# Kernel tuning notes

Measured on AMD Instinct MI355X. Metric: run time of the kernel, lower is better.

The kernel has to match this reference:

```python
import jax, jax.numpy as jnp
import numpy as np

N = 2097152
RES = 512
N_LEVELS = 6  # 512,256,128,64,32,16 (stop at LIGHT_MIN_RES=16)
MIN_ROUGHNESS = 0.08
MAX_ROUGHNESS = 0.5


def _dot(a, b):
    return jnp.sum(a * b, axis=-1, keepdims=True)


def _safe_normalize(x):
    return x / jnp.sqrt(jnp.clip(_dot(x, x), 1e-20, None))


def _reflect(x, n):
    return 2.0 * _dot(x, n) * n - x


def _rgb_to_srgb(x):
    return jnp.where(x <= 0.0031308, 12.92 * x,
                     1.055 * jnp.power(jnp.maximum(x, 0.0031308), 1.0 / 2.4) - 0.055)


def _cube_face_uv(d):
    # OpenGL / nvdiffrast cube-map convention (inverse of util.cube_to_dir)
    x, y, z = d[..., 0], d[..., 1], d[..., 2]
    ax, ay, az = jnp.abs(x), jnp.abs(y), jnp.abs(z)
    is_x = (ax >= ay) & (ax >= az)
    is_y = (~is_x) & (ay >= az)
    face = jnp.where(is_x, jnp.where(x > 0, 0, 1),
           jnp.where(is_y, jnp.where(y > 0, 2, 3),
                           jnp.where(z > 0, 4, 5)))
    ma = jnp.maximum(jnp.where(is_x, ax, jnp.where(is_y, ay, az)), 1e-20)
    u = jnp.where(is_x, jnp.where(x > 0, -z, z),
        jnp.where(is_y, x, jnp.where(z > 0, x, -x)))
    v = jnp.where(is_y, jnp.where(y > 0, z, -z), -y)
    return face, u / ma, v / ma


def _bilinear_gather(tex, face, fx, fy):
    # tex: [6,H,W,C]; face/fx/fy: [N]
    H, W = tex.shape[1], tex.shape[2]
    x0 = jnp.floor(fx); y0 = jnp.floor(fy)
    tx = (fx - x0)[:, None]; ty = (fy - y0)[:, None]
    x0i = jnp.clip(x0.astype(jnp.int32), 0, W - 1)
    x1i = jnp.clip(x0i + 1, 0, W - 1)
    y0i = jnp.clip(y0.astype(jnp.int32), 0, H - 1)
    y1i = jnp.clip(y0i + 1, 0, H - 1)
    c00 = tex[face, y0i, x0i]; c01 = tex[face, y0i, x1i]
    c10 = tex[face, y1i, x0i]; c11 = tex[face, y1i, x1i]
    return (c00 * (1 - tx) + c01 * tx) * (1 - ty) + (c10 * (1 - tx) + c11 * tx) * ty


def _sample_cubemap(tex, dirs):
    H, W = tex.shape[1], tex.shape[2]
    face, u, v = _cube_face_uv(dirs)
    return _bilinear_gather(tex, face, (u * 0.5 + 0.5) * W - 0.5, (v * 0.5 + 0.5) * H - 0.5)


def _sample_cubemap_mip(mips, dirs, level):
    # trilinear: bilinear in each of the two bracketing mip levels + lerp on level
    L = len(mips)
    samples = jnp.stack([_sample_cubemap(m, dirs) for m in mips], axis=0)  # [L,N,C]
    lvl = jnp.clip(level, 0.0, L - 1.0)
    l0 = jnp.floor(lvl).astype(jnp.int32)
    l1 = jnp.minimum(l0 + 1, L - 1)
    f = (lvl - l0.astype(lvl.dtype))[:, None]
    n = jnp.arange(dirs.shape[0])
    return samples[l0, n] * (1 - f) + samples[l1, n] * f


def _sample_lut(lut, uv):
    # lut: [H,W,C]; uv in [0,1], u -> width, v -> height, clamp boundary
    H, W = lut.shape[0], lut.shape[1]
    fx = uv[:, 0] * W - 0.5; fy = uv[:, 1] * H - 0.5
    x0 = jnp.floor(fx); y0 = jnp.floor(fy)
    tx = (fx - x0)[:, None]; ty = (fy - y0)[:, None]
    x0i = jnp.clip(x0.astype(jnp.int32), 0, W - 1); x1i = jnp.clip(x0i + 1, 0, W - 1)
    y0i = jnp.clip(y0.astype(jnp.int32), 0, H - 1); y1i = jnp.clip(y0i + 1, 0, H - 1)
    c00 = lut[y0i, x0i]; c01 = lut[y0i, x1i]; c10 = lut[y1i, x0i]; c11 = lut[y1i, x1i]
    return (c00 * (1 - tx) + c01 * tx) * (1 - ty) + (c10 * (1 - tx) + c11 * tx) * ty


def _get_mip(roughness, n_levels):
    lo = (jnp.clip(roughness, MIN_ROUGHNESS, MAX_ROUGHNESS) - MIN_ROUGHNESS) \
         / (MAX_ROUGHNESS - MIN_ROUGHNESS) * (n_levels - 2)
    hi = (jnp.clip(roughness, MAX_ROUGHNESS, 1.0) - MAX_ROUGHNESS) / (1.0 - MAX_ROUGHNESS) + n_levels - 2
    return jnp.where(roughness < MAX_ROUGHNESS, lo, hi)


def _shade(view_dir, normal, kd, ks, reflect_occ, diffuse_map, mips, fg_lut):
    roughness = ks[:, 1:2]
    metallic = ks[:, 2:3]
    spec_col = (1.0 - metallic) * 0.04 + kd * metallic
    diff_col = kd * (1.0 - metallic)
    reflvec = _safe_normalize(_reflect(view_dir, normal))
    diffuse = jnp.clip(_sample_cubemap(diffuse_map, normal), 0.0, None)
    shaded = diffuse * diff_col * (1.0 - ks[:, 0:1])
    NdotV = jnp.clip(_dot(view_dir, normal), 1e-4, None)
    fg = _sample_lut(fg_lut, jnp.concatenate([NdotV, roughness], axis=-1))
    miplevel = _get_mip(roughness[:, 0], len(mips))
    spec = jnp.clip(_sample_cubemap_mip(mips, reflvec, miplevel), 0.0, None)
    reflectance = spec_col * fg[:, 0:1] + fg[:, 1:2]
    shaded = shaded + spec * reflectance * (1.0 - reflect_occ)
    return _rgb_to_srgb(jnp.clip(shaded, 0.0, 1.0))


def setup_inputs() -> dict:
    key = jax.random.key(0)
    k = jax.random.split(key, 16)
    inp = {
        "view_dir": _safe_normalize(jax.random.normal(k[0], (N, 3), jnp.float32)),
        "normal": _safe_normalize(jax.random.normal(k[1], (N, 3), jnp.float32)),
        "kd": jax.random.uniform(k[2], (N, 3), jnp.float32),
        "ks": jax.random.uniform(k[3], (N, 3), jnp.float32),
        "reflect_occ": jax.random.uniform(k[4], (N, 1), jnp.float32),
    }
    # learned / prefiltered environment light parameters (from build_mips)
    inp["diffuse_map"] = jax.random.uniform(k[5], (6, 16, 16, 3), jnp.float32)
    res = RES
    for i in range(N_LEVELS):
        inp[f"spec{i}"] = jax.random.uniform(k[6 + i], (6, res, res, 3), jnp.float32)
        res //= 2
    inp["fg_lut"] = jax.random.uniform(k[12], (256, 256, 2), jnp.float32)
    return inp


def reference(view_dir, normal, kd, ks, reflect_occ, diffuse_map,
              spec0, spec1, spec2, spec3, spec4, spec5, fg_lut):
    mips = [spec0, spec1, spec2, spec3, spec4, spec5]
    return _shade(view_dir, normal, kd, ks, reflect_occ, diffuse_map, mips, fg_lut)
```

## Files before the change

kernel.cpp:

```cpp
#include <hip/hip_runtime.h>
#include <hip/hip_fp16.h>
#include <math.h>


typedef unsigned int u32;
typedef u32  u32x4 __attribute__((ext_vector_type(4)));
typedef float f32x4 __attribute__((ext_vector_type(4)));
struct __attribute__((packed, aligned(8))) U4p { u32x4 v; };
struct __attribute__((packed, aligned(8))) F4p { f32x4 v; };

struct CubePair {
    int iRow0, iRow1;
    bool lo;
    float w00, w01, w10, w11;
};

__device__ __forceinline__ CubePair cube_addr(int lr, float dx, float dy, float dz) {
    float ax = fabsf(dx), ay = fabsf(dy), az = fabsf(dz);
    bool is_x = (ax >= ay) && (ax >= az);
    bool is_y = (!is_x) && (ay >= az);
    int face = is_x ? (dx > 0.f ? 0 : 1)
                    : (is_y ? (dy > 0.f ? 2 : 3) : (dz > 0.f ? 4 : 5));
    float ma = fmaxf(is_x ? ax : (is_y ? ay : az), 1e-20f);
    float u = is_x ? (dx > 0.f ? -dz : dz) : (is_y ? dx : (dz > 0.f ? dx : -dx));
    float v = is_y ? (dy > 0.f ? dz : -dz) : -dy;
    float inv = __builtin_amdgcn_rcpf(ma);
    float R = (float)(1 << lr);
    float fx = (u * inv * 0.5f + 0.5f) * R - 0.5f;
    float fy = (v * inv * 0.5f + 0.5f) * R - 0.5f;
    float x0f = floorf(fx), y0f = floorf(fy);
    float tx = fx - x0f, ty = fy - y0f;
    int W = 1 << lr;
    int x0 = min(max((int)x0f, 0), W - 1);
    int y0 = min(max((int)y0f, 0), W - 1);
    int y1 = min(y0 + 1, W - 1);
    int xbase = min(x0, W - 2);
    int base = face << (2 * lr);
    CubePair a;
    a.iRow0 = base + (y0 << lr) + xbase;
    a.iRow1 = base + (y1 << lr) + xbase;
    a.lo = (x0 == xbase);
    a.w00 = (1.f - tx) * (1.f - ty);
    a.w01 = tx * (1.f - ty);
    a.w10 = (1.f - tx) * ty;
    a.w11 = tx * ty;
    return a;
}

__device__ __forceinline__ void h2f3(u32 lo, u32 hi, float& r, float& g, float& b) {
    __half2 h01 = *reinterpret_cast<__half2*>(&lo);
    float2 rg = __half22float2(h01);
    r = rg.x; g = rg.y;
    __half hb = *reinterpret_cast<__half*>(&hi);
    b = __half2float(hb);
}

__device__ __forceinline__ void gather_h(const uint2* __restrict__ tex, const CubePair& a,
                                         float& r, float& g, float& b) {
    u32x4 q0 = ((const U4p*)(tex + a.iRow0))->v;
    u32x4 q1 = ((const U4p*)(tex + a.iRow1))->v;
    u32 c00l = a.lo ? q0.x : q0.z, c00h = a.lo ? q0.y : q0.w;
    u32 c10l = a.lo ? q1.x : q1.z, c10h = a.lo ? q1.y : q1.w;
    float r00, g00, b00, r01, g01, b01, r10, g10, b10, r11, g11, b11;
    h2f3(c00l, c00h, r00, g00, b00);
    h2f3(q0.z, q0.w, r01, g01, b01);
    h2f3(c10l, c10h, r10, g10, b10);
    h2f3(q1.z, q1.w, r11, g11, b11);
    r = r00 * a.w00 + r01 * a.w01 + r10 * a.w10 + r11 * a.w11;
    g = g00 * a.w00 + g01 * a.w01 + g10 * a.w10 + g11 * a.w11;
    b = b00 * a.w00 + b01 * a.w01 + b10 * a.w10 + b11 * a.w11;
}

__device__ __forceinline__ void gather_f(const float* __restrict__ tex, const CubePair& a,
                                         float& r, float& g, float& b) {
    int i00 = a.lo ? a.iRow0 : a.iRow0 + 1;
    int i10 = a.lo ? a.iRow1 : a.iRow1 + 1;
    int i01 = a.iRow0 + 1;
    int i11 = a.iRow1 + 1;
    const float* p00 = tex + 3 * i00;
    const float* p01 = tex + 3 * i01;
    const float* p10 = tex + 3 * i10;
    const float* p11 = tex + 3 * i11;
    r = p00[0] * a.w00 + p01[0] * a.w01 + p10[0] * a.w10 + p11[0] * a.w11;
    g = p00[1] * a.w00 + p01[1] * a.w01 + p10[1] * a.w10 + p11[1] * a.w11;
    b = p00[2] * a.w00 + p01[2] * a.w01 + p10[2] * a.w10 + p11[2] * a.w11;
}

__device__ __forceinline__ float srgb1(float x) {
    float p = 1.055f * __builtin_amdgcn_exp2f(
                  __builtin_amdgcn_logf(fmaxf(x, 0.0031308f)) * (1.0f / 2.4f)) - 0.055f;
    return (x <= 0.0031308f) ? (12.92f * x) : p;
}

__global__ __launch_bounds__(256)
void repack_kernel(const float* __restrict__ src, uint2* __restrict__ dst, int ntex) {
    int i = blockIdx.x * blockDim.x + threadIdx.x;
    if (i >= ntex) return;
    float r = src[3 * i], g = src[3 * i + 1], b = src[3 * i + 2];
    __half2 rg = __floats2half2_rn(r, g);
    __half2 bz = __floats2half2_rn(b, 0.f);
    uint2 q;
    q.x = *reinterpret_cast<unsigned int*>(&rg);
    q.y = *reinterpret_cast<unsigned int*>(&bz);
    dst[i] = q;
}

template <bool PACKED, typename TexT>
__global__ __launch_bounds__(256, 4)
void envlight_kernel(const float* __restrict__ view_dir,
                     const float* __restrict__ normal,
                     const float* __restrict__ kd,
                     const float* __restrict__ ks,
                     const float* __restrict__ reflect_occ,
                     const float* __restrict__ diffuse_map,
                     const TexT* __restrict__ t0, const TexT* __restrict__ t1,
                     const TexT* __restrict__ t2, const TexT* __restrict__ t3,
                     const TexT* __restrict__ t4, const TexT* __restrict__ t5,
                     const float* __restrict__ fg_lut,
                     float* __restrict__ out, int n)
{
    __shared__ float sdiff[6 * 16 * 16 * 3];
    {
        const uint4* src4 = (const uint4*)diffuse_map;
        uint4* dst4 = (uint4*)sdiff;
        for (int k = threadIdx.x; k < 1152; k += 256)
            dst4[k] = src4[k];
    }
    __syncthreads();

    int i = blockIdx.x * blockDim.x + threadIdx.x;
    if (i >= n) return;

    float vx = view_dir[3 * i + 0], vy = view_dir[3 * i + 1], vz = view_dir[3 * i + 2];
    float nx = normal[3 * i + 0],  ny = normal[3 * i + 1],  nz = normal[3 * i + 2];
    float kdx = kd[3 * i + 0], kdy = kd[3 * i + 1], kdz = kd[3 * i + 2];
    float ks0 = ks[3 * i + 0], rough = ks[3 * i + 1], metallic = ks[3 * i + 2];
    float occ = reflect_occ[i];

    float vdotn = vx * nx + vy * ny + vz * nz;
    float rx = 2.f * vdotn * nx - vx;
    float ry = 2.f * vdotn * ny - vy;
    float rz = 2.f * vdotn * nz - vz;
    float rlen2 = fmaxf(rx * rx + ry * ry + rz * rz, 1e-20f);
    float rinv = __builtin_amdgcn_rsqf(rlen2);
    rx *= rinv; ry *= rinv; rz *= rinv;

    CubePair aDiff = cube_addr(4, nx, ny, nz);

    int lutRow0, lutRow1; bool lutLo;
    float lw00, lw01, lw10, lw11;
    {
        float NdotV = fmaxf(vdotn, 1e-4f);
        float fx = NdotV * 256.f - 0.5f;
        float fy = rough * 256.f - 0.5f;
        float x0f = floorf(fx), y0f = floorf(fy);
        float tx = fx - x0f, ty = fy - y0f;
        int x0 = min(max((int)x0f, 0), 255);
        int y0 = min(max((int)y0f, 0), 255);
        int y1 = min(y0 + 1, 255);
        int xbase = min(x0, 254);
        lutRow0 = y0 * 256 + xbase;
        lutRow1 = y1 * 256 + xbase;
        lutLo = (x0 == xbase);
        lw00 = (1.f - tx) * (1.f - ty);
        lw01 = tx * (1.f - ty);
        lw10 = (1.f - tx) * ty;
        lw11 = tx * ty;
    }

    const float MINR = 0.08f, MAXR = 0.5f;
    float lo = (fminf(fmaxf(rough, MINR), MAXR) - MINR) * (4.0f / (MAXR - MINR));
    float hi = (fminf(fmaxf(rough, MAXR), 1.0f) - MAXR) * (1.0f / (1.0f - MAXR)) + 4.0f;
    float lvl = (rough < MAXR) ? lo : hi;
    lvl = fminf(fmaxf(lvl, 0.f), 5.f);
    int l0 = min(max((int)floorf(lvl), 0), 5);
    int l1 = min(l0 + 1, 5);
    float f = lvl - (float)l0;

    const TexT* tA = (l0 == 0) ? t0 : (l0 == 1) ? t1 : (l0 == 2) ? t2
                    : (l0 == 3) ? t3 : (l0 == 4) ? t4 : t5;
    const TexT* tB = (l1 == 1) ? t1 : (l1 == 2) ? t2 : (l1 == 3) ? t3
                    : (l1 == 4) ? t4 : t5;
    CubePair aA = cube_addr(9 - l0, rx, ry, rz);
    CubePair aB = cube_addr(9 - l1, rx, ry, rz);

    float ar, ag, ab_, br, bg, bb;
    if constexpr (PACKED) {
        gather_h((const uint2*)tA, aA, ar, ag, ab_);
        gather_h((const uint2*)tB, aB, br, bg, bb);
    } else {
        gather_f((const float*)tA, aA, ar, ag, ab_);
        gather_f((const float*)tB, aB, br, bg, bb);
    }

    const float2* lut2 = (const float2*)fg_lut;
    f32x4 lq0 = ((const F4p*)(lut2 + lutRow0))->v;
    f32x4 lq1 = ((const F4p*)(lut2 + lutRow1))->v;
    float l00x = lutLo ? lq0.x : lq0.z, l00y = lutLo ? lq0.y : lq0.w;
    float l10x = lutLo ? lq1.x : lq1.z, l10y = lutLo ? lq1.y : lq1.w;
    float fg0 = l00x * lw00 + lq0.z * lw01 + l10x * lw10 + lq1.z * lw11;
    float fg1 = l00y * lw00 + lq0.w * lw01 + l10y * lw10 + lq1.w * lw11;

    int d00 = aDiff.lo ? aDiff.iRow0 : aDiff.iRow0 + 1;
    int d10 = aDiff.lo ? aDiff.iRow1 : aDiff.iRow1 + 1;
    int d01 = aDiff.iRow0 + 1;
    int d11 = aDiff.iRow1 + 1;
    float dfr = sdiff[3 * d00] * aDiff.w00 + sdiff[3 * d01] * aDiff.w01
              + sdiff[3 * d10] * aDiff.w10 + sdiff[3 * d11] * aDiff.w11;
    float dfg = sdiff[3 * d00 + 1] * aDiff.w00 + sdiff[3 * d01 + 1] * aDiff.w01
              + sdiff[3 * d10 + 1] * aDiff.w10 + sdiff[3 * d11 + 1] * aDiff.w11;
    float dfb = sdiff[3 * d00 + 2] * aDiff.w00 + sdiff[3 * d01 + 2] * aDiff.w01
              + sdiff[3 * d10 + 2] * aDiff.w10 + sdiff[3 * d11 + 2] * aDiff.w11;

    dfr = fmaxf(dfr, 0.f); dfg = fmaxf(dfg, 0.f); dfb = fmaxf(dfb, 0.f);

    float spr = fmaxf(ar * (1.f - f) + br * f, 0.f);
    float spg = fmaxf(ag * (1.f - f) + bg * f, 0.f);
    float spb = fmaxf(ab_ * (1.f - f) + bb * f, 0.f);

    float m = metallic;
    float scx = (1.f - m) * 0.04f + kdx * m;
    float scy = (1.f - m) * 0.04f + kdy * m;
    float scz = (1.f - m) * 0.04f + kdz * m;
    float dcx = kdx * (1.f - m);
    float dcy = kdy * (1.f - m);
    float dcz = kdz * (1.f - m);

    float kds = 1.f - ks0;
    float shx = dfr * dcx * kds;
    float shy = dfg * dcy * kds;
    float shz = dfb * dcz * kds;

    float om = 1.f - occ;
    shx += spr * (scx * fg0 + fg1) * om;
    shy += spg * (scy * fg0 + fg1) * om;
    shz += spb * (scz * fg0 + fg1) * om;

    out[3 * i + 0] = srgb1(fminf(fmaxf(shx, 0.f), 1.f));
    out[3 * i + 1] = srgb1(fminf(fmaxf(shy, 0.f), 1.f));
    out[3 * i + 2] = srgb1(fminf(fmaxf(shz, 0.f), 1.f));
}

extern "C" void kernel_launch(void* const* d_in, const int* in_sizes, int n_in,
                              void* d_out, int out_size, void* d_ws, size_t ws_size,
                              hipStream_t stream) {
    const float* view_dir    = (const float*)d_in[0];
    const float* normal      = (const float*)d_in[1];
    const float* kd          = (const float*)d_in[2];
    const float* ks          = (const float*)d_in[3];
    const float* reflect_occ = (const float*)d_in[4];
    const float* diffuse_map = (const float*)d_in[5];
    const float* s0          = (const float*)d_in[6];
    const float* s1          = (const float*)d_in[7];
    const float* s2          = (const float*)d_in[8];
    const float* s3          = (const float*)d_in[9];
    const float* s4          = (const float*)d_in[10];
    const float* s5          = (const float*)d_in[11];
    const float* fg_lut      = (const float*)d_in[12];
    float* out = (float*)d_out;

    int n = in_sizes[0] / 3;
    int block = 256;
    int grid = (n + block - 1) / block;

    static const int NT[6]  = {1572864, 393216, 98304, 24576, 6144, 1536};
    static const int OFF[6] = {0, 1572864, 1966080, 2064384, 2088960, 2095104};
    const size_t NEED = 2096640ull * 8;

    if (ws_size >= NEED) {
        uint2* packed = (uint2*)d_ws;
        const float* srcs[6] = {s0, s1, s2, s3, s4, s5};
        for (int l = 0; l < 6; ++l) {
            int nt = NT[l];
            repack_kernel<<<(nt + 255) / 256, 256, 0, stream>>>(srcs[l], packed + OFF[l], nt);
        }
        envlight_kernel<true, uint2><<<grid, block, 0, stream>>>(
            view_dir, normal, kd, ks, reflect_occ, diffuse_map,
            packed + OFF[0], packed + OFF[1], packed + OFF[2],
            packed + OFF[3], packed + OFF[4], packed + OFF[5],
            fg_lut, out, n);
    } else {
        envlight_kernel<false, float><<<grid, block, 0, stream>>>(
            view_dir, normal, kd, ks, reflect_occ, diffuse_map,
            s0, s1, s2, s3, s4, s5, fg_lut, out, n);
    }
}
```

Before: 251.3 us.

## Repack textures into 2x2-quad RGB9E5 texels for single-load bilinear fetch

```diff
diff --git a/kernel.cpp b/kernel.cpp
--- a/kernel.cpp
+++ b/kernel.cpp
@@ -9,13 +9,249 @@
 struct __attribute__((packed, aligned(8))) U4p { u32x4 v; };
 struct __attribute__((packed, aligned(8))) F4p { f32x4 v; };
 
+__device__ __forceinline__ u32 enc9e5(float r, float g, float b) {
+    r = fminf(fmaxf(r, 0.f), 65408.f);
+    g = fminf(fmaxf(g, 0.f), 65408.f);
+    b = fminf(fmaxf(b, 0.f), 65408.f);
+    float maxc = fmaxf(r, fmaxf(g, b));
+    int e = ((__float_as_int(maxc) >> 23) & 0xff) - 127;
+    int exp_p = max(e + 16, 0);
+    float denom = __int_as_float((exp_p + 103) << 23);
+    int maxm = (int)(maxc / denom + 0.5f);
+    if (maxm == 512) { exp_p += 1; denom *= 2.f; }
+    float rd = 1.f / denom;
+    u32 rm = (u32)(r * rd + 0.5f);
+    u32 gm = (u32)(g * rd + 0.5f);
+    u32 bm = (u32)(b * rd + 0.5f);
+    return rm | (gm << 9) | (bm << 18) | ((u32)exp_p << 27);
+}
+
+__device__ __forceinline__ void dec9e5_acc(u32 pk, float w, float& r, float& g, float& b) {
+    float scale = __int_as_float((int)(((pk >> 27) & 31u) + 103u) << 23) * w;
+    r += (float)(pk & 511u) * scale;
+    g += (float)((pk >> 9) & 511u) * scale;
+    b += (float)((pk >> 18) & 511u) * scale;
+}
+
+struct CubeQ { int idx; float w00, w01, w10, w11; };
+
+__device__ __forceinline__ CubeQ cube_addr_q(int lr, float dx, float dy, float dz) {
+    float ax = fabsf(dx), ay = fabsf(dy), az = fabsf(dz);
+    bool is_x = (ax >= ay) && (ax >= az);
+    bool is_y = (!is_x) && (ay >= az);
+    int face = is_x ? (dx > 0.f ? 0 : 1)
+                    : (is_y ? (dy > 0.f ? 2 : 3) : (dz > 0.f ? 4 : 5));
+    float ma = fmaxf(is_x ? ax : (is_y ? ay : az), 1e-20f);
+    float u = is_x ? (dx > 0.f ? -dz : dz) : (is_y ? dx : (dz > 0.f ? dx : -dx));
+    float v = is_y ? (dy > 0.f ? dz : -dz) : -dy;
+    float inv = __builtin_amdgcn_rcpf(ma);
+    float R = (float)(1 << lr);
+    float fx = (u * inv * 0.5f + 0.5f) * R - 0.5f;
+    float fy = (v * inv * 0.5f + 0.5f) * R - 0.5f;
+    float x0f = floorf(fx), y0f = floorf(fy);
+    float tx = fx - x0f, ty = fy - y0f;
+    int W = 1 << lr;
+    int x0 = min(max((int)x0f, 0), W - 1);
+    int y0 = min(max((int)y0f, 0), W - 1);
+    CubeQ a;
+    a.idx = (face << (2 * lr)) + (y0 << lr) + x0;
+    a.w00 = (1.f - tx) * (1.f - ty);
+    a.w01 = tx * (1.f - ty);
+    a.w10 = (1.f - tx) * ty;
+    a.w11 = tx * ty;
+    return a;
+}
+
+__device__ __forceinline__ void gather_q9(uint4 q, const CubeQ& a,
+                                          float& r, float& g, float& b) {
+    r = 0.f; g = 0.f; b = 0.f;
+    dec9e5_acc(q.x, a.w00, r, g, b);
+    dec9e5_acc(q.y, a.w01, r, g, b);
+    dec9e5_acc(q.z, a.w10, r, g, b);
+    dec9e5_acc(q.w, a.w11, r, g, b);
+}
+
+__device__ __forceinline__ float srgb1(float x) {
+    float p = 1.055f * __builtin_amdgcn_exp2f(
+                  __builtin_amdgcn_logf(fmaxf(x, 0.0031308f)) * (1.0f / 2.4f)) - 0.055f;
+    return (x <= 0.0031308f) ? (12.92f * x) : p;
+}
+
+__global__ __launch_bounds__(256)
+void repack_q9(const float* __restrict__ src, uint4* __restrict__ dst, int lr, int ntex) {
+    int i = blockIdx.x * blockDim.x + threadIdx.x;
+    if (i >= ntex) return;
+    int W = 1 << lr;
+    int face = i >> (2 * lr);
+    int rem = i & (W * W - 1);
+    int y = rem >> lr, x = rem & (W - 1);
+    int x1 = min(x + 1, W - 1), y1 = min(y + 1, W - 1);
+    int base = face << (2 * lr);
+    int i00 = 3 * (base + (y << lr) + x);
+    int i01 = 3 * (base + (y << lr) + x1);
+    int i10 = 3 * (base + (y1 << lr) + x);
+    int i11 = 3 * (base + (y1 << lr) + x1);
+    uint4 q;
+    q.x = enc9e5(src[i00], src[i00 + 1], src[i00 + 2]);
+    q.y = enc9e5(src[i01], src[i01 + 1], src[i01 + 2]);
+    q.z = enc9e5(src[i10], src[i10 + 1], src[i10 + 2]);
+    q.w = enc9e5(src[i11], src[i11 + 1], src[i11 + 2]);
+    dst[i] = q;
+}
+
+__global__ __launch_bounds__(256)
+void repack_lutq(const float2* __restrict__ lut, uint4* __restrict__ dst) {
+    int i = blockIdx.x * blockDim.x + threadIdx.x;
+    if (i >= 65536) return;
+    int y = i >> 8, x = i & 255;
+    int x1 = min(x + 1, 255), y1 = min(y + 1, 255);
+    float2 c00 = lut[(y << 8) + x],  c01 = lut[(y << 8) + x1];
+    float2 c10 = lut[(y1 << 8) + x], c11 = lut[(y1 << 8) + x1];
+    __half2 h00 = __floats2half2_rn(c00.x, c00.y);
+    __half2 h01 = __floats2half2_rn(c01.x, c01.y);
+    __half2 h10 = __floats2half2_rn(c10.x, c10.y);
+    __half2 h11 = __floats2half2_rn(c11.x, c11.y);
+    uint4 q;
+    q.x = *reinterpret_cast<u32*>(&h00);
+    q.y = *reinterpret_cast<u32*>(&h01);
+    q.z = *reinterpret_cast<u32*>(&h10);
+    q.w = *reinterpret_cast<u32*>(&h11);
+    dst[i] = q;
+}
+
+__global__ __launch_bounds__(256)
+void repack_pair(const float* __restrict__ src, uint2* __restrict__ dst, int ntex) {
+    int i = blockIdx.x * blockDim.x + threadIdx.x;
+    if (i >= ntex) return;
+    float r = src[3 * i], g = src[3 * i + 1], b = src[3 * i + 2];
+    __half2 rg = __floats2half2_rn(r, g);
+    __half2 bz = __floats2half2_rn(b, 0.f);
+    uint2 q;
+    q.x = *reinterpret_cast<u32*>(&rg);
+    q.y = *reinterpret_cast<u32*>(&bz);
+    dst[i] = q;
+}
+
+__global__ __launch_bounds__(256)
+void envlight_quad(const float* __restrict__ view_dir,
+                   const float* __restrict__ normal,
+                   const float* __restrict__ kd,
+                   const float* __restrict__ ks,
+                   const float* __restrict__ reflect_occ,
+                   const uint4* __restrict__ dquad,
+                   const uint4* __restrict__ t0, const uint4* __restrict__ t1,
+                   const uint4* __restrict__ t2, const uint4* __restrict__ t3,
+                   const uint4* __restrict__ t4, const uint4* __restrict__ t5,
+                   const uint4* __restrict__ lutq,
+                   float* __restrict__ out, int n)
+{
+    int i = blockIdx.x * blockDim.x + threadIdx.x;
+    if (i >= n) return;
+
+    float vx = view_dir[3 * i + 0], vy = view_dir[3 * i + 1], vz = view_dir[3 * i + 2];
+    float nx = normal[3 * i + 0],  ny = normal[3 * i + 1],  nz = normal[3 * i + 2];
+    float kdx = kd[3 * i + 0], kdy = kd[3 * i + 1], kdz = kd[3 * i + 2];
+    float ks0 = ks[3 * i + 0], rough = ks[3 * i + 1], metallic = ks[3 * i + 2];
+    float occ = reflect_occ[i];
+
+    float vdotn = vx * nx + vy * ny + vz * nz;
+    float rx = 2.f * vdotn * nx - vx;
+    float ry = 2.f * vdotn * ny - vy;
+    float rz = 2.f * vdotn * nz - vz;
+    float rlen2 = fmaxf(rx * rx + ry * ry + rz * rz, 1e-20f);
+    float rinv = __builtin_amdgcn_rsqf(rlen2);
+    rx *= rinv; ry *= rinv; rz *= rinv;
+
+    CubeQ aDiff = cube_addr_q(4, nx, ny, nz);
+
+    int lutIdx; float lw00, lw01, lw10, lw11;
+    {
+        float NdotV = fmaxf(vdotn, 1e-4f);
+        float fx = NdotV * 256.f - 0.5f;
+        float fy = rough * 256.f - 0.5f;
+        float x0f = floorf(fx), y0f = floorf(fy);
+        float tx = fx - x0f, ty = fy - y0f;
+        int x0 = min(max((int)x0f, 0), 255);
+        int y0 = min(max((int)y0f, 0), 255);
+        lutIdx = (y0 << 8) + x0;
+        lw00 = (1.f - tx) * (1.f - ty);
+        lw01 = tx * (1.f - ty);
+        lw10 = (1.f - tx) * ty;
+        lw11 = tx * ty;
+    }
+
+    const float MINR = 0.08f, MAXR = 0.5f;
+    float lo = (fminf(fmaxf(rough, MINR), MAXR) - MINR) * (4.0f / (MAXR - MINR));
+    float hi = (fminf(fmaxf(rough, MAXR), 1.0f) - MAXR) * (1.0f / (1.0f - MAXR)) + 4.0f;
+    float lvl = (rough < MAXR) ? lo : hi;
+    lvl = fminf(fmaxf(lvl, 0.f), 5.f);
+    int l0 = min(max((int)floorf(lvl), 0), 5);
+    int l1 = min(l0 + 1, 5);
+    float f = lvl - (float)l0;
+
+    const uint4* tA = (l0 == 0) ? t0 : (l0 == 1) ? t1 : (l0 == 2) ? t2
+                     : (l0 == 3) ? t3 : (l0 == 4) ? t4 : t5;
+    const uint4* tB = (l1 == 1) ? t1 : (l1 == 2) ? t2 : (l1 == 3) ? t3
+                     : (l1 == 4) ? t4 : t5;
+    CubeQ aA = cube_addr_q(9 - l0, rx, ry, rz);
+    CubeQ aB = cube_addr_q(9 - l1, rx, ry, rz);
+
+    uint4 qA = tA[aA.idx];
+    uint4 qB = tB[aB.idx];
+    uint4 lq = lutq[lutIdx];
+    uint4 dq = dquad[aDiff.idx];
+
+    float ar, ag, ab_, br, bg, bb;
+    gather_q9(qA, aA, ar, ag, ab_);
+    gather_q9(qB, aB, br, bg, bb);
+
+    __half2 h00 = *reinterpret_cast<__half2*>(&lq.x);
+    __half2 h01 = *reinterpret_cast<__half2*>(&lq.y);
+    __half2 h10 = *reinterpret_cast<__half2*>(&lq.z);
+    __half2 h11 = *reinterpret_cast<__half2*>(&lq.w);
+    float2 c00 = __half22float2(h00), c01 = __half22float2(h01);
+    float2 c10 = __half22float2(h10), c11 = __half22float2(h11);
+    float fg0 = c00.x * lw00 + c01.x * lw01 + c10.x * lw10 + c11.x * lw11;
+    float fg1 = c00.y * lw00 + c01.y * lw01 + c10.y * lw10 + c11.y * lw11;
+
+    float dfr, dfg, dfb;
+    gather_q9(dq, aDiff, dfr, dfg, dfb);
+    dfr = fmaxf(dfr, 0.f); dfg = fmaxf(dfg, 0.f); dfb = fmaxf(dfb, 0.f);
+
+    float spr = fmaxf(ar * (1.f - f) + br * f, 0.f);
+    float spg = fmaxf(ag * (1.f - f) + bg * f, 0.f);
+    float spb = fmaxf(ab_ * (1.f - f) + bb * f, 0.f);
+
+    float m = metallic;
+    float scx = (1.f - m) * 0.04f + kdx * m;
+    float scy = (1.f - m) * 0.04f + kdy * m;
+    float scz = (1.f - m) * 0.04f + kdz * m;
+    float dcx = kdx * (1.f - m);
+    float dcy = kdy * (1.f - m);
+    float dcz = kdz * (1.f - m);
+
+    float kds = 1.f - ks0;
+    float shx = dfr * dcx * kds;
+    float shy = dfg * dcy * kds;
+    float shz = dfb * dcz * kds;
+
+    float om = 1.f - occ;
+    shx += spr * (scx * fg0 + fg1) * om;
+    shy += spg * (scy * fg0 + fg1) * om;
+    shz += spb * (scz * fg0 + fg1) * om;
+
+    out[3 * i + 0] = srgb1(fminf(fmaxf(shx, 0.f), 1.f));
+    out[3 * i + 1] = srgb1(fminf(fmaxf(shy, 0.f), 1.f));
+    out[3 * i + 2] = srgb1(fminf(fmaxf(shz, 0.f), 1.f));
+}
+
 struct CubePair {
     int iRow0, iRow1;
     bool lo;
     float w00, w01, w10, w11;
 };
 
-__device__ __forceinline__ CubePair cube_addr(int lr, float dx, float dy, float dz) {
+__device__ __forceinline__ CubePair cube_addr_p(int lr, float dx, float dy, float dz) {
     float ax = fabsf(dx), ay = fabsf(dy), az = fabsf(dz);
     bool is_x = (ax >= ay) && (ax >= az);
     bool is_y = (!is_x) && (ay >= az);
@@ -55,8 +291,8 @@
     b = __half2float(hb);
 }
 
-__device__ __forceinline__ void gather_h(const uint2* __restrict__ tex, const CubePair& a,
-                                         float& r, float& g, float& b) {
+__device__ __forceinline__ void gather_hp(const uint2* __restrict__ tex, const CubePair& a,
+                                          float& r, float& g, float& b) {
     u32x4 q0 = ((const U4p*)(tex + a.iRow0))->v;
     u32x4 q1 = ((const U4p*)(tex + a.iRow1))->v;
     u32 c00l = a.lo ? q0.x : q0.z, c00h = a.lo ? q0.y : q0.w;
@@ -71,53 +307,18 @@
     b = b00 * a.w00 + b01 * a.w01 + b10 * a.w10 + b11 * a.w11;
 }
 
-__device__ __forceinline__ void gather_f(const float* __restrict__ tex, const CubePair& a,
-                                         float& r, float& g, float& b) {
-    int i00 = a.lo ? a.iRow0 : a.iRow0 + 1;
-    int i10 = a.lo ? a.iRow1 : a.iRow1 + 1;
-    int i01 = a.iRow0 + 1;
-    int i11 = a.iRow1 + 1;
-    const float* p00 = tex + 3 * i00;
-    const float* p01 = tex + 3 * i01;
-    const float* p10 = tex + 3 * i10;
-    const float* p11 = tex + 3 * i11;
-    r = p00[0] * a.w00 + p01[0] * a.w01 + p10[0] * a.w10 + p11[0] * a.w11;
-    g = p00[1] * a.w00 + p01[1] * a.w01 + p10[1] * a.w10 + p11[1] * a.w11;
-    b = p00[2] * a.w00 + p01[2] * a.w01 + p10[2] * a.w10 + p11[2] * a.w11;
-}
-
-__device__ __forceinline__ float srgb1(float x) {
-    float p = 1.055f * __builtin_amdgcn_exp2f(
-                  __builtin_amdgcn_logf(fmaxf(x, 0.0031308f)) * (1.0f / 2.4f)) - 0.055f;
-    return (x <= 0.0031308f) ? (12.92f * x) : p;
-}
-
-__global__ __launch_bounds__(256)
-void repack_kernel(const float* __restrict__ src, uint2* __restrict__ dst, int ntex) {
-    int i = blockIdx.x * blockDim.x + threadIdx.x;
-    if (i >= ntex) return;
-    float r = src[3 * i], g = src[3 * i + 1], b = src[3 * i + 2];
-    __half2 rg = __floats2half2_rn(r, g);
-    __half2 bz = __floats2half2_rn(b, 0.f);
-    uint2 q;
-    q.x = *reinterpret_cast<unsigned int*>(&rg);
-    q.y = *reinterpret_cast<unsigned int*>(&bz);
-    dst[i] = q;
-}
-
-template <bool PACKED, typename TexT>
 __global__ __launch_bounds__(256, 4)
-void envlight_kernel(const float* __restrict__ view_dir,
-                     const float* __restrict__ normal,
-                     const float* __restrict__ kd,
-                     const float* __restrict__ ks,
-                     const float* __restrict__ reflect_occ,
-                     const float* __restrict__ diffuse_map,
-                     const TexT* __restrict__ t0, const TexT* __restrict__ t1,
-                     const TexT* __restrict__ t2, const TexT* __restrict__ t3,
-                     const TexT* __restrict__ t4, const TexT* __restrict__ t5,
-                     const float* __restrict__ fg_lut,
-                     float* __restrict__ out, int n)
+void envlight_pair(const float* __restrict__ view_dir,
+                   const float* __restrict__ normal,
+                   const float* __restrict__ kd,
+                   const float* __restrict__ ks,
+                   const float* __restrict__ reflect_occ,
+                   const float* __restrict__ diffuse_map,
+                   const uint2* __restrict__ t0, const uint2* __restrict__ t1,
+                   const uint2* __restrict__ t2, const uint2* __restrict__ t3,
+                   const uint2* __restrict__ t4, const uint2* __restrict__ t5,
+                   const float* __restrict__ fg_lut,
+                   float* __restrict__ out, int n)
 {
     __shared__ float sdiff[6 * 16 * 16 * 3];
     {
@@ -145,7 +346,7 @@
     float rinv = __builtin_amdgcn_rsqf(rlen2);
     rx *= rinv; ry *= rinv; rz *= rinv;
 
-    CubePair aDiff = cube_addr(4, nx, ny, nz);
+    CubePair aDiff = cube_addr_p(4, nx, ny, nz);
 
     int lutRow0, lutRow1; bool lutLo;
     float lw00, lw01, lw10, lw11;
@@ -159,8 +360,8 @@
         int y0 = min(max((int)y0f, 0), 255);
         int y1 = min(y0 + 1, 255);
         int xbase = min(x0, 254);
-        lutRow0 = y0 * 256 + xbase;
-        lutRow1 = y1 * 256 + xbase;
+        lutRow0 = (y0 << 8) + xbase;
+        lutRow1 = (y1 << 8) + xbase;
         lutLo = (x0 == xbase);
         lw00 = (1.f - tx) * (1.f - ty);
         lw01 = tx * (1.f - ty);
@@ -177,21 +378,16 @@
     int l1 = min(l0 + 1, 5);
     float f = lvl - (float)l0;
 
-    const TexT* tA = (l0 == 0) ? t0 : (l0 == 1) ? t1 : (l0 == 2) ? t2
-                    : (l0 == 3) ? t3 : (l0 == 4) ? t4 : t5;
-    const TexT* tB = (l1 == 1) ? t1 : (l1 == 2) ? t2 : (l1 == 3) ? t3
-                    : (l1 == 4) ? t4 : t5;
-    CubePair aA = cube_addr(9 - l0, rx, ry, rz);
-    CubePair aB = cube_addr(9 - l1, rx, ry, rz);
+    const uint2* tA = (l0 == 0) ? t0 : (l0 == 1) ? t1 : (l0 == 2) ? t2
+                     : (l0 == 3) ? t3 : (l0 == 4) ? t4 : t5;
+    const uint2* tB = (l1 == 1) ? t1 : (l1 == 2) ? t2 : (l1 == 3) ? t3
+                     : (l1 == 4) ? t4 : t5;
+    CubePair aA = cube_addr_p(9 - l0, rx, ry, rz);
+    CubePair aB = cube_addr_p(9 - l1, rx, ry, rz);
 
     float ar, ag, ab_, br, bg, bb;
-    if constexpr (PACKED) {
-        gather_h((const uint2*)tA, aA, ar, ag, ab_);
-        gather_h((const uint2*)tB, aB, br, bg, bb);
-    } else {
-        gather_f((const float*)tA, aA, ar, ag, ab_);
-        gather_f((const float*)tB, aB, br, bg, bb);
-    }
+    gather_hp(tA, aA, ar, ag, ab_);
+    gather_hp(tB, aB, br, bg, bb);
 
     const float2* lut2 = (const float2*)fg_lut;
     f32x4 lq0 = ((const F4p*)(lut2 + lutRow0))->v;
@@ -265,23 +461,36 @@
 
     static const int NT[6]  = {1572864, 393216, 98304, 24576, 6144, 1536};
     static const int OFF[6] = {0, 1572864, 1966080, 2064384, 2088960, 2095104};
-    const size_t NEED = 2096640ull * 8;
-
-    if (ws_size >= NEED) {
-        uint2* packed = (uint2*)d_ws;
-        const float* srcs[6] = {s0, s1, s2, s3, s4, s5};
+    const int SPEC_TOTAL = 2096640;
+    const int LUT_OFF = SPEC_TOTAL;
+    const int DIF_OFF = SPEC_TOTAL + 65536;
+    const size_t NEED_Q = (size_t)(SPEC_TOTAL + 65536 + 1536) * 16;
+    const size_t NEED_P = 2096640ull * 8;
+
+    const float* srcs[6] = {s0, s1, s2, s3, s4, s5};
+
+    if (ws_size >= NEED_Q) {
+        uint4* q = (uint4*)d_ws;
         for (int l = 0; l < 6; ++l) {
             int nt = NT[l];
-            repack_kernel<<<(nt + 255) / 256, 256, 0, stream>>>(srcs[l], packed + OFF[l], nt);
+            repack_q9<<<(nt + 255) / 256, 256, 0, stream>>>(srcs[l], q + OFF[l], 9 - l, nt);
         }
-        envlight_kernel<true, uint2><<<grid, block, 0, stream>>>(
+        repack_q9<<<(1536 + 255) / 256, 256, 0, stream>>>(diffuse_map, q + DIF_OFF, 4, 1536);
+        repack_lutq<<<65536 / 256, 256, 0, stream>>>((const float2*)fg_lut, q + LUT_OFF);
+        envlight_quad<<<grid, block, 0, stream>>>(
+            view_dir, normal, kd, ks, reflect_occ, q + DIF_OFF,
+            q + OFF[0], q + OFF[1], q + OFF[2], q + OFF[3], q + OFF[4], q + OFF[5],
+            q + LUT_OFF, out, n);
+    } else {
+        uint2* packed = (uint2*)d_ws;
+        for (int l = 0; l < 6; ++l) {
+            int nt = NT[l];
+            repack_pair<<<(nt + 255) / 256, 256, 0, stream>>>(srcs[l], packed + OFF[l], nt);
+        }
+        envlight_pair<<<grid, block, 0, stream>>>(
             view_dir, normal, kd, ks, reflect_occ, diffuse_map,
             packed + OFF[0], packed + OFF[1], packed + OFF[2],
             packed + OFF[3], packed + OFF[4], packed + OFF[5],
             fg_lut, out, n);
-    } else {
-        envlight_kernel<false, float><<<grid, block, 0, stream>>>(
-            view_dir, normal, kd, ks, reflect_occ, diffuse_map,
-            s0, s1, s2, s3, s4, s5, fg_lut, out, n);
     }
 }
```

Measured after the change: 247.9 us. About the same (-1.3%).
